# Kernel optimization log

Measured on AMD Instinct MI355X. Metric: run time of the kernel, lower is better.

Reference implementation:

```python
import jax, jax.numpy as jnp
import numpy as np

TOP_K = 2
EPS = 1e-10


def setup_inputs() -> dict:
    key = jax.random.key(0)
    k1, k2 = jax.random.split(key)
    B, S, D, E = 4, 4096, 4096, 64
    hidden_states = jax.random.normal(k1, (B, S, D), dtype=jnp.float32)
    # router weight, scaled like a standard linear init
    w_router = jax.random.normal(k2, (D, E), dtype=jnp.float32) / np.sqrt(D)
    return {"hidden_states": hidden_states, "w_router": w_router}


def reference(hidden_states, w_router):
    # router: [B,S,D] x [D,E] -> [B,S,E]
    router_logits = jnp.einsum("bsd,de->bse", hidden_states, w_router)
    # balanced_assignment: softmax, global load, penalty, adjusted top-k
    routing_probs = jax.nn.softmax(router_logits, axis=-1)
    current_load = routing_probs.sum(axis=(0, 1))            # [E]
    load_penalty = current_load / (current_load.mean() + EPS)  # [E]
    adjusted_logits = router_logits - jnp.log(load_penalty + EPS)
    _, expert_indices = jax.lax.top_k(adjusted_logits, TOP_K)  # [B,S,top_k]
    return adjusted_logits, expert_indices
```

## Files before the change

kernel.cpp:

```cpp
#include <hip/hip_runtime.h>
#include <math.h>

#define ROWS 16384
#define DD   4096
#define EE   64
#define EPSF 1e-10f

#define BM    64
#define KT    64
#define NKT   (DD / KT)
#define WTILE 8192
#define BTILE (2 * WTILE)

typedef __attribute__((ext_vector_type(8))) short short8;
typedef __attribute__((ext_vector_type(4))) float f32x4;
typedef __attribute__((ext_vector_type(4))) unsigned u32x4;

__device__ __forceinline__ void split2x8(const float f[8], u32x4& w0,
                                         u32x4& w1) {
#pragma unroll
  for (int i = 0; i < 4; ++i) {
    float fa = f[2 * i], fb = f[2 * i + 1];
    unsigned ua = __float_as_uint(fa), ub = __float_as_uint(fb);
    unsigned ra = ua + 0x7fffu + ((ua >> 16) & 1u);
    unsigned rb = ub + 0x7fffu + ((ub >> 16) & 1u);
    w0[i] = (rb & 0xffff0000u) | (ra >> 16);
    fa -= __uint_as_float(ra & 0xffff0000u);
    fb -= __uint_as_float(rb & 0xffff0000u);
    ua = __float_as_uint(fa); ub = __float_as_uint(fb);
    ra = ua + 0x7fffu + ((ua >> 16) & 1u);
    rb = ub + 0x7fffu + ((ub >> 16) & 1u);
    w1[i] = (rb & 0xffff0000u) | (ra >> 16);
  }
}

__device__ __forceinline__ void dma16(const void* g, void* l) {
  __builtin_amdgcn_global_load_lds(
      (const __attribute__((address_space(1))) unsigned int*)g,
      (__attribute__((address_space(3))) unsigned int*)l, 16, 0, 0);
}

__global__ __launch_bounds__(256) void k_wsplit(const float* __restrict__ wr,
                                                unsigned char* __restrict__ out,
                                                float* __restrict__ g_load) {
  const int kt = blockIdx.x;
  const int t = threadIdx.x;
  const int lane = t & 63, wv = t >> 6;
  if (blockIdx.x == 0 && t < 64) g_load[t] = 0.f;
  float f[8];
  const float* wp = wr + (size_t)(kt * 32 + wv * 8) * EE + lane;
#pragma unroll
  for (int j = 0; j < 8; ++j) f[j] = wp[(size_t)j * EE];
  u32x4 w0, w1;
  split2x8(f, w0, w1);
  const int et = lane >> 4;
  const int lp = wv * 16 + (lane & 15);
  unsigned char* base = out + (size_t)kt * WTILE + et * 1024 + lp * 16;
  *(u32x4*)(base + 0 * 4096) = w0;
  *(u32x4*)(base + 1 * 4096) = w1;
}

__global__ __launch_bounds__(512) void k_gemm(
    const float* __restrict__ h, const unsigned char* __restrict__ wsp,
    float* __restrict__ logits, float* __restrict__ g_load) {
  __shared__ alignas(16) unsigned char smem[2 * BTILE];

  const int t = threadIdx.x;
  const int lane = t & 63;
  const int wv = t >> 6;
  const int mt = wv >> 1;
  const int sub = wv & 1;
  const int row0 = blockIdx.x * BM;

  f32x4 acc[4] = {};

  const float* ap = h + (size_t)(row0 + mt * 16 + (lane & 15)) * DD +
                    sub * 32 + (lane >> 4) * 8;
  const int dmaoff = t * 16;

  float4 c0, c1, n0, n1;

#pragma unroll
  for (int i = 0; i < 2; ++i)
    dma16(wsp + i * 8192 + dmaoff, smem + i * 8192 + dmaoff);
  c0 = *(const float4*)(ap);
  c1 = *(const float4*)(ap + 4);

  for (int kt = 0; kt < NKT; ++kt) {
    const int buf = kt & 1;
    asm volatile("s_waitcnt vmcnt(0)" ::: "memory");
    __syncthreads();

    if (kt + 1 < NKT) {
      const unsigned char* ws = wsp + (size_t)(kt + 1) * BTILE;
      unsigned char* nb = smem + (buf ^ 1) * BTILE;
#pragma unroll
      for (int i = 0; i < 2; ++i)
        dma16(ws + i * 8192 + dmaoff, nb + i * 8192 + dmaoff);
      const float* p = ap + (size_t)(kt + 1) * KT;
      n0 = *(const float4*)(p);
      n1 = *(const float4*)(p + 4);
    }

    const unsigned char* lb = smem + buf * BTILE + sub * WTILE;
    short8 bf[2][4];
#pragma unroll
    for (int p = 0; p < 2; ++p)
#pragma unroll
      for (int e = 0; e < 4; ++e)
        bf[p][e] = *(const short8*)&lb[p * 4096 + e * 1024 + lane * 16];

    const float af[8] = {c0.x, c0.y, c0.z, c0.w, c1.x, c1.y, c1.z, c1.w};
    u32x4 q0, q1;
    split2x8(af, q0, q1);
    const short8 ah0 = __builtin_bit_cast(short8, q0);
    const short8 ah1 = __builtin_bit_cast(short8, q1);
#pragma unroll
    for (int e = 0; e < 4; ++e) {
      f32x4 c = acc[e];
      c = __builtin_amdgcn_mfma_f32_16x16x32_bf16(ah0, bf[0][e], c, 0, 0, 0);
      c = __builtin_amdgcn_mfma_f32_16x16x32_bf16(ah0, bf[1][e], c, 0, 0, 0);
      c = __builtin_amdgcn_mfma_f32_16x16x32_bf16(ah1, bf[0][e], c, 0, 0, 0);
      acc[e] = c;
    }

    if (kt + 1 < NKT) { c0 = n0; c1 = n1; }
  }

  asm volatile("s_waitcnt vmcnt(0)" ::: "memory");
  __syncthreads();
  float* sl = (float*)smem;
  {
    const int rb = mt * 16 + (lane >> 4) * 4;
    const int cb = lane & 15;
    if (sub == 0) {
#pragma unroll
      for (int e = 0; e < 4; ++e)
#pragma unroll
        for (int r = 0; r < 4; ++r)
          sl[(rb + r) * 68 + e * 16 + cb] = acc[e][r];
    }
    __syncthreads();
    if (sub == 1) {
#pragma unroll
      for (int e = 0; e < 4; ++e)
#pragma unroll
        for (int r = 0; r < 4; ++r)
          sl[(rb + r) * 68 + e * 16 + cb] += acc[e][r];
    }
    __syncthreads();
  }

  float accp = 0.f;
#pragma unroll
  for (int i = 0; i < 8; ++i) {
    const int row = wv * 8 + i;
    const float x = sl[row * 68 + lane];
    float m = x;
#pragma unroll
    for (int off = 32; off > 0; off >>= 1) m = fmaxf(m, __shfl_xor(m, off, 64));
    const float p = __expf(x - m);
    float s = p;
#pragma unroll
    for (int off = 32; off > 0; off >>= 1) s += __shfl_xor(s, off, 64);
    accp += p / s;
    logits[(size_t)(row0 + row) * EE + lane] = x;
  }
  float* red = sl + 64 * 68;
  red[wv * 64 + lane] = accp;
  __syncthreads();
  if (wv == 0) {
    float s = 0.f;
#pragma unroll
    for (int j = 0; j < 8; ++j) s += red[j * 64 + lane];
    atomicAdd(&g_load[lane], s);
  }
}

__global__ __launch_bounds__(256) void k_top2(float* __restrict__ logits,
                                              const float* __restrict__ g_load,
                                              float* __restrict__ idx_out) {
  int t = threadIdx.x;
  int lane = t & 63;
  int wv = t >> 6;
  int row = blockIdx.x * 4 + wv;

  float v0 = g_load[lane];
  float s0 = v0;
#pragma unroll
  for (int off = 32; off > 0; off >>= 1) s0 += __shfl_xor(s0, off, 64);
  float lp = logf(v0 / (s0 * (1.f / 64.f) + EPSF) + EPSF);

  size_t base = (size_t)row * EE;
  float a = logits[base + lane] - lp;
  logits[base + lane] = a;

  float v = a;
  int idx = lane;
#pragma unroll
  for (int off = 32; off > 0; off >>= 1) {
    float ov = __shfl_xor(v, off, 64);
    int oi = __shfl_xor(idx, off, 64);
    if (ov > v || (ov == v && oi < idx)) { v = ov; idx = oi; }
  }
  int i1 = idx;

  float a2 = (lane == i1) ? -INFINITY : a;
  v = a2;
  idx = lane;
#pragma unroll
  for (int off = 32; off > 0; off >>= 1) {
    float ov = __shfl_xor(v, off, 64);
    int oi = __shfl_xor(idx, off, 64);
    if (ov > v || (ov == v && oi < idx)) { v = ov; idx = oi; }
  }
  int i2 = idx;

  if (lane == 0) {
    idx_out[(size_t)row * 2 + 0] = (float)i1;
    idx_out[(size_t)row * 2 + 1] = (float)i2;
  }
}

extern "C" void kernel_launch(void* const* d_in, const int* in_sizes, int n_in,
                              void* d_out, int out_size, void* d_ws,
                              size_t ws_size, hipStream_t stream) {
  const float* h = (const float*)d_in[0];
  const float* wr = (const float*)d_in[1];
  float* out = (float*)d_out;
  float* logits = out;
  float* idx_out = out + (size_t)ROWS * EE;
  float* g_load = (float*)d_ws;
  unsigned char* wsp = (unsigned char*)d_ws + 512;

  k_wsplit<<<DD / 32, 256, 0, stream>>>(wr, wsp, g_load);
  k_gemm<<<ROWS / BM, 512, 0, stream>>>(h, wsp, logits, g_load);
  k_top2<<<ROWS / 4, 256, 0, stream>>>(logits, g_load, idx_out);
}
```

Baseline: 399.2 us.

## Split GEMM K dimension across two blocks with atomic accumulation

```diff
diff --git a/kernel.cpp b/kernel.cpp
--- a/kernel.cpp
+++ b/kernel.cpp
@@ -6,11 +6,13 @@
 #define EE   64
 #define EPSF 1e-10f
 
-#define BM    64
-#define KT    64
-#define NKT   (DD / KT)
-#define WTILE 8192
-#define BTILE (2 * WTILE)
+#define BM     64
+#define KSPLIT 2
+#define KRANGE (DD / KSPLIT)
+#define KT     64
+#define NPH    (KRANGE / KT)
+#define WTILE  8192
+#define BTILE  (2 * WTILE)
 
 typedef __attribute__((ext_vector_type(8))) short short8;
 typedef __attribute__((ext_vector_type(4))) float f32x4;
@@ -62,7 +64,7 @@
 
 __global__ __launch_bounds__(512) void k_gemm(
     const float* __restrict__ h, const unsigned char* __restrict__ wsp,
-    float* __restrict__ logits, float* __restrict__ g_load) {
+    float* __restrict__ logits) {
   __shared__ alignas(16) unsigned char smem[2 * BTILE];
 
   const int t = threadIdx.x;
@@ -70,29 +72,31 @@
   const int wv = t >> 6;
   const int mt = wv >> 1;
   const int sub = wv & 1;
-  const int row0 = blockIdx.x * BM;
+  const int row0 = (blockIdx.x >> 1) * BM;
+  const int ks = blockIdx.x & 1;
 
   f32x4 acc[4] = {};
 
   const float* ap = h + (size_t)(row0 + mt * 16 + (lane & 15)) * DD +
-                    sub * 32 + (lane >> 4) * 8;
+                    ks * KRANGE + sub * 32 + (lane >> 4) * 8;
+  const unsigned char* wbase = wsp + (size_t)ks * NPH * BTILE;
   const int dmaoff = t * 16;
 
   float4 c0, c1, n0, n1;
 
 #pragma unroll
   for (int i = 0; i < 2; ++i)
-    dma16(wsp + i * 8192 + dmaoff, smem + i * 8192 + dmaoff);
+    dma16(wbase + i * 8192 + dmaoff, smem + i * 8192 + dmaoff);
   c0 = *(const float4*)(ap);
   c1 = *(const float4*)(ap + 4);
 
-  for (int kt = 0; kt < NKT; ++kt) {
+  for (int kt = 0; kt < NPH; ++kt) {
     const int buf = kt & 1;
     asm volatile("s_waitcnt vmcnt(0)" ::: "memory");
     __syncthreads();
 
-    if (kt + 1 < NKT) {
-      const unsigned char* ws = wsp + (size_t)(kt + 1) * BTILE;
+    if (kt + 1 < NPH) {
+      const unsigned char* ws = wbase + (size_t)(kt + 1) * BTILE;
       unsigned char* nb = smem + (buf ^ 1) * BTILE;
 #pragma unroll
       for (int i = 0; i < 2; ++i)
@@ -124,55 +128,42 @@
       acc[e] = c;
     }
 
-    if (kt + 1 < NKT) { c0 = n0; c1 = n1; }
-  }
-
-  asm volatile("s_waitcnt vmcnt(0)" ::: "memory");
-  __syncthreads();
-  float* sl = (float*)smem;
-  {
-    const int rb = mt * 16 + (lane >> 4) * 4;
-    const int cb = lane & 15;
-    if (sub == 0) {
-#pragma unroll
-      for (int e = 0; e < 4; ++e)
-#pragma unroll
-        for (int r = 0; r < 4; ++r)
-          sl[(rb + r) * 68 + e * 16 + cb] = acc[e][r];
-    }
-    __syncthreads();
-    if (sub == 1) {
-#pragma unroll
-      for (int e = 0; e < 4; ++e)
-#pragma unroll
-        for (int r = 0; r < 4; ++r)
-          sl[(rb + r) * 68 + e * 16 + cb] += acc[e][r];
-    }
-    __syncthreads();
-  }
-
+    if (kt + 1 < NPH) { c0 = n0; c1 = n1; }
+  }
+
+  const int rbase = row0 + mt * 16 + (lane >> 4) * 4;
+  const int col = lane & 15;
+#pragma unroll
+  for (int e = 0; e < 4; ++e)
+#pragma unroll
+    for (int r = 0; r < 4; ++r)
+      atomicAdd(&logits[(size_t)(rbase + r) * EE + e * 16 + col],
+                acc[e][r]);
+}
+
+__global__ __launch_bounds__(256) void k_softload(
+    const float* __restrict__ logits, float* __restrict__ g_load) {
+  __shared__ float red[4][64];
+  const int lane = threadIdx.x & 63;
+  const int wv = threadIdx.x >> 6;
   float accp = 0.f;
-#pragma unroll
-  for (int i = 0; i < 8; ++i) {
-    const int row = wv * 8 + i;
-    const float x = sl[row * 68 + lane];
+#pragma unroll 4
+  for (int i = 0; i < 16; ++i) {
+    int row = blockIdx.x * 64 + wv * 16 + i;
+    float x = logits[(size_t)row * EE + lane];
     float m = x;
 #pragma unroll
     for (int off = 32; off > 0; off >>= 1) m = fmaxf(m, __shfl_xor(m, off, 64));
-    const float p = __expf(x - m);
+    float p = __expf(x - m);
     float s = p;
 #pragma unroll
     for (int off = 32; off > 0; off >>= 1) s += __shfl_xor(s, off, 64);
     accp += p / s;
-    logits[(size_t)(row0 + row) * EE + lane] = x;
-  }
-  float* red = sl + 64 * 68;
-  red[wv * 64 + lane] = accp;
+  }
+  red[wv][lane] = accp;
   __syncthreads();
   if (wv == 0) {
-    float s = 0.f;
-#pragma unroll
-    for (int j = 0; j < 8; ++j) s += red[j * 64 + lane];
+    float s = red[0][lane] + red[1][lane] + red[2][lane] + red[3][lane];
     atomicAdd(&g_load[lane], s);
   }
 }
@@ -233,7 +224,9 @@
   float* g_load = (float*)d_ws;
   unsigned char* wsp = (unsigned char*)d_ws + 512;
 
+  hipMemsetAsync(logits, 0, (size_t)ROWS * EE * sizeof(float), stream);
   k_wsplit<<<DD / 32, 256, 0, stream>>>(wr, wsp, g_load);
-  k_gemm<<<ROWS / BM, 512, 0, stream>>>(h, wsp, logits, g_load);
+  k_gemm<<<(ROWS / BM) * KSPLIT, 512, 0, stream>>>(h, wsp, logits);
+  k_softload<<<ROWS / 64, 256, 0, stream>>>(logits, g_load);
   k_top2<<<ROWS / 4, 256, 0, stream>>>(logits, g_load, idx_out);
 }
```

After: 404.6 us. Within noise of the previous version (+1.4%).

## Load split weights directly to registers and deepen A prefetch pipeline

Applied to the files above, without the earlier changes.

```diff
diff --git a/kernel.cpp b/kernel.cpp
--- a/kernel.cpp
+++ b/kernel.cpp
@@ -7,10 +7,8 @@
 #define EPSF 1e-10f
 
 #define BM    64
-#define KT    64
-#define NKT   (DD / KT)
+#define NS    (DD / 32 / 2)
 #define WTILE 8192
-#define BTILE (2 * WTILE)
 
 typedef __attribute__((ext_vector_type(8))) short short8;
 typedef __attribute__((ext_vector_type(4))) float f32x4;
@@ -34,12 +32,6 @@
   }
 }
 
-__device__ __forceinline__ void dma16(const void* g, void* l) {
-  __builtin_amdgcn_global_load_lds(
-      (const __attribute__((address_space(1))) unsigned int*)g,
-      (__attribute__((address_space(3))) unsigned int*)l, 16, 0, 0);
-}
-
 __global__ __launch_bounds__(256) void k_wsplit(const float* __restrict__ wr,
                                                 unsigned char* __restrict__ out,
                                                 float* __restrict__ g_load) {
@@ -63,7 +55,7 @@
 __global__ __launch_bounds__(512) void k_gemm(
     const float* __restrict__ h, const unsigned char* __restrict__ wsp,
     float* __restrict__ logits, float* __restrict__ g_load) {
-  __shared__ alignas(16) unsigned char smem[2 * BTILE];
+  __shared__ float sl[64 * 68 + 8 * 64];
 
   const int t = threadIdx.x;
   const int lane = t & 63;
@@ -76,41 +68,38 @@
 
   const float* ap = h + (size_t)(row0 + mt * 16 + (lane & 15)) * DD +
                     sub * 32 + (lane >> 4) * 8;
-  const int dmaoff = t * 16;
-
-  float4 c0, c1, n0, n1;
-
-#pragma unroll
-  for (int i = 0; i < 2; ++i)
-    dma16(wsp + i * 8192 + dmaoff, smem + i * 8192 + dmaoff);
-  c0 = *(const float4*)(ap);
-  c1 = *(const float4*)(ap + 4);
-
-  for (int kt = 0; kt < NKT; ++kt) {
-    const int buf = kt & 1;
-    asm volatile("s_waitcnt vmcnt(0)" ::: "memory");
-    __syncthreads();
-
-    if (kt + 1 < NKT) {
-      const unsigned char* ws = wsp + (size_t)(kt + 1) * BTILE;
-      unsigned char* nb = smem + (buf ^ 1) * BTILE;
-#pragma unroll
-      for (int i = 0; i < 2; ++i)
-        dma16(ws + i * 8192 + dmaoff, nb + i * 8192 + dmaoff);
-      const float* p = ap + (size_t)(kt + 1) * KT;
-      n0 = *(const float4*)(p);
-      n1 = *(const float4*)(p + 4);
-    }
-
-    const unsigned char* lb = smem + buf * BTILE + sub * WTILE;
-    short8 bf[2][4];
-#pragma unroll
-    for (int p = 0; p < 2; ++p)
-#pragma unroll
-      for (int e = 0; e < 4; ++e)
-        bf[p][e] = *(const short8*)&lb[p * 4096 + e * 1024 + lane * 16];
-
-    const float af[8] = {c0.x, c0.y, c0.z, c0.w, c1.x, c1.y, c1.z, c1.w};
+  const unsigned char* wb = wsp + sub * (size_t)WTILE + lane * 16;
+
+  float4 ac0, ac1, am0, am1, an0, an1;
+  short8 bc[2][4], bn[2][4];
+
+  ac0 = *(const float4*)(ap);
+  ac1 = *(const float4*)(ap + 4);
+  am0 = *(const float4*)(ap + 64);
+  am1 = *(const float4*)(ap + 68);
+#pragma unroll
+  for (int p = 0; p < 2; ++p)
+#pragma unroll
+    for (int e = 0; e < 4; ++e)
+      bc[p][e] = *(const short8*)(wb + p * 4096 + e * 1024);
+
+  for (int kt = 0; kt < NS; ++kt) {
+    if (kt + 1 < NS) {
+      const unsigned char* wn = wb + (size_t)(kt + 1) * 16384;
+#pragma unroll
+      for (int p = 0; p < 2; ++p)
+#pragma unroll
+        for (int e = 0; e < 4; ++e)
+          bn[p][e] = *(const short8*)(wn + p * 4096 + e * 1024);
+    }
+    if (kt + 2 < NS) {
+      const float* p4 = ap + (size_t)(kt + 2) * 64;
+      an0 = *(const float4*)(p4);
+      an1 = *(const float4*)(p4 + 4);
+    }
+
+    const float af[8] = {ac0.x, ac0.y, ac0.z, ac0.w,
+                         ac1.x, ac1.y, ac1.z, ac1.w};
     u32x4 q0, q1;
     split2x8(af, q0, q1);
     const short8 ah0 = __builtin_bit_cast(short8, q0);
@@ -118,18 +107,19 @@
 #pragma unroll
     for (int e = 0; e < 4; ++e) {
       f32x4 c = acc[e];
-      c = __builtin_amdgcn_mfma_f32_16x16x32_bf16(ah0, bf[0][e], c, 0, 0, 0);
-      c = __builtin_amdgcn_mfma_f32_16x16x32_bf16(ah0, bf[1][e], c, 0, 0, 0);
-      c = __builtin_amdgcn_mfma_f32_16x16x32_bf16(ah1, bf[0][e], c, 0, 0, 0);
+      c = __builtin_amdgcn_mfma_f32_16x16x32_bf16(ah0, bc[0][e], c, 0, 0, 0);
+      c = __builtin_amdgcn_mfma_f32_16x16x32_bf16(ah0, bc[1][e], c, 0, 0, 0);
+      c = __builtin_amdgcn_mfma_f32_16x16x32_bf16(ah1, bc[0][e], c, 0, 0, 0);
       acc[e] = c;
     }
 
-    if (kt + 1 < NKT) { c0 = n0; c1 = n1; }
-  }
-
-  asm volatile("s_waitcnt vmcnt(0)" ::: "memory");
-  __syncthreads();
-  float* sl = (float*)smem;
+    ac0 = am0; ac1 = am1; am0 = an0; am1 = an1;
+#pragma unroll
+    for (int p = 0; p < 2; ++p)
+#pragma unroll
+      for (int e = 0; e < 4; ++e) bc[p][e] = bn[p][e];
+  }
+
   {
     const int rb = mt * 16 + (lane >> 4) * 4;
     const int cb = lane & 15;
```

Measured after the change: 405.7 us. About the same (+1.6%).
